# Optimization experiments

Hardware: AMD Instinct MI355X
Metric: run time of the kernel (lower is better)

## Reference

```python
import jax, jax.numpy as jnp
import numpy as np

N_NODES = 100000
N_EDGES = 1600000
D_HID = 64  # per-party hidden width; concat of two parties -> 128


def setup_inputs() -> dict:
    key = jax.random.key(0)
    k1, k2, k3, k4, k5 = jax.random.split(key, 5)
    h1 = jax.random.normal(k1, (N_NODES, D_HID), dtype=jnp.float32)
    h2 = jax.random.normal(k2, (N_NODES, D_HID), dtype=jnp.float32)
    # Glorot-ish scale for dense layers
    W1 = jax.random.normal(k3, (2 * 2 * D_HID, 16), dtype=jnp.float32) * (1.0 / np.sqrt(2 * 2 * D_HID))
    b1 = jnp.zeros((16,), dtype=jnp.float32)
    W2 = jax.random.normal(k4, (16, 1), dtype=jnp.float32) * 0.25
    b2 = jnp.zeros((1,), dtype=jnp.float32)
    edges = jax.random.randint(k5, (2, N_EDGES), 0, N_NODES, dtype=jnp.int64)
    return {"h1": h1, "h2": h2, "W1": W1, "b1": b1, "W2": W2, "b2": b2, "edges": edges}


def reference(h1, h2, W1, b1, W2, b2, edges):
    # concat party hiddens -> node features [N, 128]
    x = jnp.concatenate([h1, h2], axis=-1)
    src, dst = edges[0], edges[1]
    # gather + concat -> edge representations [E, 256]
    edge_rep = jnp.concatenate([x[src], x[dst]], axis=-1)
    h = edge_rep @ W1 + b1          # [E, 16] (Dense(16), linear activation)
    logits = h @ W2 + b2            # [E, 1]  (Dense(1))
    return logits
```

## Files before the change

### kernel.cpp

```cpp
#include <hip/hip_runtime.h>

#define N_NODES 100000
#define N_EDGES 1600000


__global__ void prep_kernel(const float* __restrict__ W1, const float* __restrict__ b1,
                            const float* __restrict__ W2, const float* __restrict__ b2,
                            const int* __restrict__ edges32,
                            float* __restrict__ wf, float* __restrict__ cflag) {
    int t = threadIdx.x;
    float acc = 0.f;
#pragma unroll
    for (int k = 0; k < 16; ++k) acc += W1[t * 16 + k] * W2[k];
    wf[t] = acc;

    __shared__ int nz;
    if (t == 0) nz = 0;
    __syncthreads();
    if (edges32[2 * t + 1] != 0) atomicAdd(&nz, 1);
    __syncthreads();
    if (t == 0) {
        float c = b2[0];
#pragma unroll
        for (int k = 0; k < 16; ++k) c += b1[k] * W2[k];
        cflag[0] = c;
        ((int*)cflag)[1] = (nz == 0) ? 1 : 0;
    }
}

__global__ void node_kernel(const float* __restrict__ h1, const float* __restrict__ h2,
                            const float* __restrict__ wf,
                            float* __restrict__ ssrc, float* __restrict__ sdst) {
    const int li = threadIdx.x & 15;
    const int g  = threadIdx.x >> 4;
    const int node = blockIdx.x * 16 + g;

    const float4* wf4 = (const float4*)wf;
    const float4 ws1 = wf4[li];
    const float4 ws2 = wf4[16 + li];
    const float4 wd1 = wf4[32 + li];
    const float4 wd2 = wf4[48 + li];

    const float4 a = ((const float4*)(h1 + (size_t)node * 64))[li];
    const float4 b = ((const float4*)(h2 + (size_t)node * 64))[li];

    float ps = a.x * ws1.x + a.y * ws1.y + a.z * ws1.z + a.w * ws1.w
             + b.x * ws2.x + b.y * ws2.y + b.z * ws2.z + b.w * ws2.w;
    float pd = a.x * wd1.x + a.y * wd1.y + a.z * wd1.z + a.w * wd1.w
             + b.x * wd2.x + b.y * wd2.y + b.z * wd2.z + b.w * wd2.w;

#pragma unroll
    for (int off = 1; off < 16; off <<= 1) {
        ps += __shfl_xor(ps, off);
        pd += __shfl_xor(pd, off);
    }
    if (li == 0) { ssrc[node] = ps; sdst[node] = pd; }
}

__global__ void edge_kernel(const void* __restrict__ edges,
                            const float* __restrict__ ssrc, const float* __restrict__ sdst,
                            const float* __restrict__ cflag,
                            float* __restrict__ out) {
    const int e = blockIdx.x * blockDim.x + threadIdx.x;
    const float c = cflag[0];
    const int is64 = ((const int*)cflag)[1];
    int s, d;
    if (is64) {
        const long long* e64 = (const long long*)edges;
        s = (int)e64[e];
        d = (int)e64[N_EDGES + e];
    } else {
        const int* e32 = (const int*)edges;
        s = e32[e];
        d = e32[N_EDGES + e];
    }
    out[e] = ssrc[s] + sdst[d] + c;
}

extern "C" void kernel_launch(void* const* d_in, const int* in_sizes, int n_in,
                              void* d_out, int out_size, void* d_ws, size_t ws_size,
                              hipStream_t stream) {
    const float* h1 = (const float*)d_in[0];
    const float* h2 = (const float*)d_in[1];
    const float* W1 = (const float*)d_in[2];
    const float* b1 = (const float*)d_in[3];
    const float* W2 = (const float*)d_in[4];
    const float* b2 = (const float*)d_in[5];
    const void*  edges = d_in[6];

    float* wsf   = (float*)d_ws;
    float* wf    = wsf;
    float* cflag = wsf + 256;
    float* ssrc  = wsf + 512;
    float* sdst  = wsf + 512 + N_NODES;
    float* out   = (float*)d_out;

    prep_kernel<<<1, 256, 0, stream>>>(W1, b1, W2, b2, (const int*)edges, wf, cflag);
    node_kernel<<<N_NODES / 16, 256, 0, stream>>>(h1, h2, wf, ssrc, sdst);
    edge_kernel<<<N_EDGES / 256, 256, 0, stream>>>(edges, ssrc, sdst, cflag, out);
}
```

Measured before the change: 34.88 us.

## Fuse prep, node and edge passes into one cooperative kernel with grid sync

```diff
diff --git a/kernel.cpp b/kernel.cpp
--- a/kernel.cpp
+++ b/kernel.cpp
@@ -1,76 +1,126 @@
 #include <hip/hip_runtime.h>
+#include <hip/hip_cooperative_groups.h>
+
+namespace cg = cooperative_groups;
 
 #define N_NODES 100000
 #define N_EDGES 1600000
+#define GRID    1024
+#define BLOCK   256
+#define NTHR    (GRID * BLOCK)
 
-
-__global__ void prep_kernel(const float* __restrict__ W1, const float* __restrict__ b1,
-                            const float* __restrict__ W2, const float* __restrict__ b2,
-                            const int* __restrict__ edges32,
-                            float* __restrict__ wf, float* __restrict__ cflag) {
-    int t = threadIdx.x;
-    float acc = 0.f;
+__device__ __forceinline__ float fold_c(const float* __restrict__ b1,
+                                        const float* __restrict__ W2,
+                                        const float* __restrict__ b2) {
+    float c = b2[0];
 #pragma unroll
-    for (int k = 0; k < 16; ++k) acc += W1[t * 16 + k] * W2[k];
-    wf[t] = acc;
-
-    __shared__ int nz;
-    if (t == 0) nz = 0;
-    __syncthreads();
-    if (edges32[2 * t + 1] != 0) atomicAdd(&nz, 1);
-    __syncthreads();
-    if (t == 0) {
-        float c = b2[0];
-#pragma unroll
-        for (int k = 0; k < 16; ++k) c += b1[k] * W2[k];
-        cflag[0] = c;
-        ((int*)cflag)[1] = (nz == 0) ? 1 : 0;
-    }
+    for (int k = 0; k < 16; ++k) c += b1[k] * W2[k];
+    return c;
 }
 
-__global__ void node_kernel(const float* __restrict__ h1, const float* __restrict__ h2,
-                            const float* __restrict__ wf,
-                            float* __restrict__ ssrc, float* __restrict__ sdst) {
-    const int li = threadIdx.x & 15;
-    const int g  = threadIdx.x >> 4;
-    const int node = blockIdx.x * 16 + g;
+__device__ __forceinline__ bool detect_is64(const int* __restrict__ e32, int t) {
+    int w = e32[2 * (t & 63) + 1];
+    unsigned long long m = __ballot(w != 0);
+    return m == 0ULL;
+}
 
+__device__ __forceinline__ void node_pass(const float* __restrict__ h1,
+                                          const float* __restrict__ h2,
+                                          const float* __restrict__ wf,
+                                          float* __restrict__ ssrc, float* __restrict__ sdst,
+                                          int t, int bid, int nblocks) {
+    const int li = t & 15;
+    const int g  = t >> 4;
     const float4* wf4 = (const float4*)wf;
     const float4 ws1 = wf4[li];
     const float4 ws2 = wf4[16 + li];
     const float4 wd1 = wf4[32 + li];
     const float4 wd2 = wf4[48 + li];
 
-    const float4 a = ((const float4*)(h1 + (size_t)node * 64))[li];
-    const float4 b = ((const float4*)(h2 + (size_t)node * 64))[li];
+    for (int node = bid * 16 + g; node < N_NODES; node += nblocks * 16) {
+        const float4 a = ((const float4*)(h1 + (size_t)node * 64))[li];
+        const float4 b = ((const float4*)(h2 + (size_t)node * 64))[li];
+        float ps = a.x * ws1.x + a.y * ws1.y + a.z * ws1.z + a.w * ws1.w
+                 + b.x * ws2.x + b.y * ws2.y + b.z * ws2.z + b.w * ws2.w;
+        float pd = a.x * wd1.x + a.y * wd1.y + a.z * wd1.z + a.w * wd1.w
+                 + b.x * wd2.x + b.y * wd2.y + b.z * wd2.z + b.w * wd2.w;
+#pragma unroll
+        for (int off = 1; off < 16; off <<= 1) {
+            ps += __shfl_xor(ps, off);
+            pd += __shfl_xor(pd, off);
+        }
+        if (li == 0) { ssrc[node] = ps; sdst[node] = pd; }
+    }
+}
 
-    float ps = a.x * ws1.x + a.y * ws1.y + a.z * ws1.z + a.w * ws1.w
-             + b.x * ws2.x + b.y * ws2.y + b.z * ws2.z + b.w * ws2.w;
-    float pd = a.x * wd1.x + a.y * wd1.y + a.z * wd1.z + a.w * wd1.w
-             + b.x * wd2.x + b.y * wd2.y + b.z * wd2.z + b.w * wd2.w;
+__global__ void fused_kernel(const float* __restrict__ h1, const float* __restrict__ h2,
+                             const float* __restrict__ W1, const float* __restrict__ b1,
+                             const float* __restrict__ W2, const float* __restrict__ b2,
+                             const void* __restrict__ edges,
+                             float* __restrict__ ssrc, float* __restrict__ sdst,
+                             float* __restrict__ out) {
+    __shared__ float wf[256];
+    const int t = threadIdx.x;
+    {
+        float acc = 0.f;
+#pragma unroll
+        for (int k = 0; k < 16; ++k) acc += W1[t * 16 + k] * W2[k];
+        wf[t] = acc;
+    }
+    const float c = fold_c(b1, W2, b2);
+    const int* e32 = (const int*)edges;
+    const bool is64 = detect_is64(e32, t);
+    __syncthreads();
 
+    node_pass(h1, h2, wf, ssrc, sdst, t, blockIdx.x, GRID);
+
+    cg::this_grid().sync();
+
+    const int tid = blockIdx.x * BLOCK + t;
+    if (is64) {
+        const long long* e64 = (const long long*)edges;
+        for (int e = tid; e < N_EDGES; e += NTHR) {
+            int s = (int)e64[e];
+            int d = (int)e64[N_EDGES + e];
+            out[e] = ssrc[s] + sdst[d] + c;
+        }
+    } else {
+        for (int e = tid; e < N_EDGES; e += NTHR) {
+            int s = e32[e];
+            int d = e32[N_EDGES + e];
+            out[e] = ssrc[s] + sdst[d] + c;
+        }
+    }
+}
+
+__global__ void node_kernel(const float* __restrict__ h1, const float* __restrict__ h2,
+                            const float* __restrict__ W1, const float* __restrict__ W2,
+                            float* __restrict__ ssrc, float* __restrict__ sdst) {
+    __shared__ float wf[256];
+    const int t = threadIdx.x;
+    float acc = 0.f;
 #pragma unroll
-    for (int off = 1; off < 16; off <<= 1) {
-        ps += __shfl_xor(ps, off);
-        pd += __shfl_xor(pd, off);
-    }
-    if (li == 0) { ssrc[node] = ps; sdst[node] = pd; }
+    for (int k = 0; k < 16; ++k) acc += W1[t * 16 + k] * W2[k];
+    wf[t] = acc;
+    __syncthreads();
+    node_pass(h1, h2, wf, ssrc, sdst, t, blockIdx.x, gridDim.x);
 }
 
 __global__ void edge_kernel(const void* __restrict__ edges,
                             const float* __restrict__ ssrc, const float* __restrict__ sdst,
-                            const float* __restrict__ cflag,
+                            const float* __restrict__ b1, const float* __restrict__ W2,
+                            const float* __restrict__ b2,
                             float* __restrict__ out) {
     const int e = blockIdx.x * blockDim.x + threadIdx.x;
-    const float c = cflag[0];
-    const int is64 = ((const int*)cflag)[1];
+    const float c = fold_c(b1, W2, b2);
+    const int* e32 = (const int*)edges;
+    const bool is64 = detect_is64(e32, threadIdx.x);
     int s, d;
     if (is64) {
         const long long* e64 = (const long long*)edges;
         s = (int)e64[e];
         d = (int)e64[N_EDGES + e];
     } else {
-        const int* e32 = (const int*)edges;
         s = e32[e];
         d = e32[N_EDGES + e];
     }
@@ -88,14 +138,16 @@
     const float* b2 = (const float*)d_in[5];
     const void*  edges = d_in[6];
 
-    float* wsf   = (float*)d_ws;
-    float* wf    = wsf;
-    float* cflag = wsf + 256;
-    float* ssrc  = wsf + 512;
-    float* sdst  = wsf + 512 + N_NODES;
-    float* out   = (float*)d_out;
+    float* ssrc = (float*)d_ws;
+    float* sdst = ssrc + N_NODES;
+    float* out  = (float*)d_out;
 
-    prep_kernel<<<1, 256, 0, stream>>>(W1, b1, W2, b2, (const int*)edges, wf, cflag);
-    node_kernel<<<N_NODES / 16, 256, 0, stream>>>(h1, h2, wf, ssrc, sdst);
-    edge_kernel<<<N_EDGES / 256, 256, 0, stream>>>(edges, ssrc, sdst, cflag, out);
+    void* args[] = {(void*)&h1, (void*)&h2, (void*)&W1, (void*)&b1, (void*)&W2,
+                    (void*)&b2, (void*)&edges, (void*)&ssrc, (void*)&sdst, (void*)&out};
+    hipError_t err = hipLaunchCooperativeKernel((void*)fused_kernel, dim3(GRID), dim3(BLOCK),
+                                                args, 0, stream);
+    if (err != hipSuccess) {
+        node_kernel<<<N_NODES / 16, 256, 0, stream>>>(h1, h2, W1, W2, ssrc, sdst);
+        edge_kernel<<<N_EDGES / 256, 256, 0, stream>>>(edges, ssrc, sdst, b1, W2, b2, out);
+    }
 }
```

Measured after the change: 109.2 us. 213% more time.

## Fold prep kernel into node and edge kernels, process two edges per thread

Applied to the files above, without the earlier changes.

```diff
diff --git a/kernel.cpp b/kernel.cpp
--- a/kernel.cpp
+++ b/kernel.cpp
@@ -3,36 +3,22 @@
 #define N_NODES 100000
 #define N_EDGES 1600000
 
+__global__ __launch_bounds__(256) void node_kernel(
+        const float* __restrict__ h1, const float* __restrict__ h2,
+        const float* __restrict__ W1, const float* __restrict__ W2,
+        float* __restrict__ ssrc, float* __restrict__ sdst) {
+    __shared__ float wf[256];
+    const int t = threadIdx.x;
+    {
+        float acc = 0.f;
+#pragma unroll
+        for (int k = 0; k < 16; ++k) acc += W1[t * 16 + k] * W2[k];
+        wf[t] = acc;
+    }
+    __syncthreads();
 
-__global__ void prep_kernel(const float* __restrict__ W1, const float* __restrict__ b1,
-                            const float* __restrict__ W2, const float* __restrict__ b2,
-                            const int* __restrict__ edges32,
-                            float* __restrict__ wf, float* __restrict__ cflag) {
-    int t = threadIdx.x;
-    float acc = 0.f;
-#pragma unroll
-    for (int k = 0; k < 16; ++k) acc += W1[t * 16 + k] * W2[k];
-    wf[t] = acc;
-
-    __shared__ int nz;
-    if (t == 0) nz = 0;
-    __syncthreads();
-    if (edges32[2 * t + 1] != 0) atomicAdd(&nz, 1);
-    __syncthreads();
-    if (t == 0) {
-        float c = b2[0];
-#pragma unroll
-        for (int k = 0; k < 16; ++k) c += b1[k] * W2[k];
-        cflag[0] = c;
-        ((int*)cflag)[1] = (nz == 0) ? 1 : 0;
-    }
-}
-
-__global__ void node_kernel(const float* __restrict__ h1, const float* __restrict__ h2,
-                            const float* __restrict__ wf,
-                            float* __restrict__ ssrc, float* __restrict__ sdst) {
-    const int li = threadIdx.x & 15;
-    const int g  = threadIdx.x >> 4;
+    const int li = t & 15;
+    const int g  = t >> 4;
     const int node = blockIdx.x * 16 + g;
 
     const float4* wf4 = (const float4*)wf;
@@ -57,24 +43,43 @@
     if (li == 0) { ssrc[node] = ps; sdst[node] = pd; }
 }
 
-__global__ void edge_kernel(const void* __restrict__ edges,
-                            const float* __restrict__ ssrc, const float* __restrict__ sdst,
-                            const float* __restrict__ cflag,
-                            float* __restrict__ out) {
-    const int e = blockIdx.x * blockDim.x + threadIdx.x;
-    const float c = cflag[0];
-    const int is64 = ((const int*)cflag)[1];
-    int s, d;
+__global__ __launch_bounds__(256) void edge_kernel(
+        const void* __restrict__ edges,
+        const float* __restrict__ ssrc, const float* __restrict__ sdst,
+        const float* __restrict__ b1, const float* __restrict__ W2,
+        const float* __restrict__ b2,
+        float* __restrict__ out) {
+    const int t   = threadIdx.x;
+    const int tid = blockIdx.x * 256 + t;
+
+    float c = b2[0];
+#pragma unroll
+    for (int k = 0; k < 16; ++k) c += b1[k] * W2[k];
+
+    const int* e32 = (const int*)edges;
+    const bool is64 = (__ballot(e32[2 * (t & 63) + 1] != 0) == 0ULL);
+
+    int s0, d0, s1, d1;
     if (is64) {
-        const long long* e64 = (const long long*)edges;
-        s = (int)e64[e];
-        d = (int)e64[N_EDGES + e];
+        const long2* es = (const long2*)edges;
+        const long2* ed = es + (N_EDGES / 2);
+        long2 se = es[tid];
+        long2 de = ed[tid];
+        s0 = (int)se.x; s1 = (int)se.y;
+        d0 = (int)de.x; d1 = (int)de.y;
     } else {
-        const int* e32 = (const int*)edges;
-        s = e32[e];
-        d = e32[N_EDGES + e];
+        const int2* es = (const int2*)edges;
+        const int2* ed = es + (N_EDGES / 2);
+        int2 se = es[tid];
+        int2 de = ed[tid];
+        s0 = se.x; s1 = se.y;
+        d0 = de.x; d1 = de.y;
     }
-    out[e] = ssrc[s] + sdst[d] + c;
+
+    float2 r;
+    r.x = ssrc[s0] + sdst[d0] + c;
+    r.y = ssrc[s1] + sdst[d1] + c;
+    ((float2*)out)[tid] = r;
 }
 
 extern "C" void kernel_launch(void* const* d_in, const int* in_sizes, int n_in,
@@ -88,14 +93,10 @@
     const float* b2 = (const float*)d_in[5];
     const void*  edges = d_in[6];
 
-    float* wsf   = (float*)d_ws;
-    float* wf    = wsf;
-    float* cflag = wsf + 256;
-    float* ssrc  = wsf + 512;
-    float* sdst  = wsf + 512 + N_NODES;
-    float* out   = (float*)d_out;
+    float* ssrc = (float*)d_ws;
+    float* sdst = ssrc + N_NODES;
+    float* out  = (float*)d_out;
 
-    prep_kernel<<<1, 256, 0, stream>>>(W1, b1, W2, b2, (const int*)edges, wf, cflag);
-    node_kernel<<<N_NODES / 16, 256, 0, stream>>>(h1, h2, wf, ssrc, sdst);
-    edge_kernel<<<N_EDGES / 256, 256, 0, stream>>>(edges, ssrc, sdst, cflag, out);
+    node_kernel<<<N_NODES / 16, 256, 0, stream>>>(h1, h2, W1, W2, ssrc, sdst);
+    edge_kernel<<<N_EDGES / 512, 256, 0, stream>>>(edges, ssrc, sdst, b1, W2, b2, out);
 }
```

New measurement: 32.17 us. -7.8%, faster.
